# Performance work log

Measured on AMD Instinct MI355X. Metric: run time of the kernel, lower is better.

Reference implementation:

```python
import jax, jax.numpy as jnp
import numpy as np

B, H, N, F = 64, 24, 32, 256

def setup_inputs() -> dict:
    key = jax.random.key(0)
    ks = jax.random.split(key, 6)
    s = 1.0 / np.sqrt(F)
    return {
        "Q": jax.random.normal(ks[0], (B, N, F), jnp.float32),
        "K": jax.random.normal(ks[1], (B, H, N, F), jnp.float32),
        "V": jax.random.normal(ks[2], (B, H, N, F), jnp.float32),
        "Wq": jax.random.normal(ks[3], (N, F, F), jnp.float32) * s,
        "bq": jnp.zeros((N, F), jnp.float32),
        "Wk": jax.random.normal(ks[4], (N, H, F, F), jnp.float32) * s,
        "bk": jnp.zeros((N, H, F), jnp.float32),
        "Wv": jax.random.normal(ks[5], (N, H, F, F), jnp.float32) * s,
        "bv": jnp.zeros((N, H, F), jnp.float32),
    }

def reference(Q, K, V, Wq, bq, Wk, bk, Wv, bv):
    # Per-node query projection: [B,N,F]
    QWq = jnp.einsum('bnf,nfg->bng', Q, Wq) + bq
    # Per-node, per-encoder-step key/value projections: [B,N,H,F]
    KWk = jnp.einsum('bhnf,nhfg->bnhg', K, Wk) + bk
    VWv = jnp.einsum('bhnf,nhfg->bnhg', V, Wv) + bv
    # Attention scores over the H encoder steps (no sqrt(F) scaling, as in source)
    logits = jnp.einsum('bng,bnhg->bnh', QWq, KWk)
    scores = jax.nn.softmax(logits, axis=-1)          # [B,N,H]
    heads = jnp.einsum('bnh,bnhg->bng', scores, VWv)  # [B,N,F]
    return heads, scores
```

## Files before the change

### kernel.cpp

```cpp
#include <hip/hip_runtime.h>

typedef __attribute__((ext_vector_type(8))) short short8;
typedef __attribute__((ext_vector_type(4))) float f32x4;

#define B_ 64
#define H_ 24
#define N_ 32
#define F_ 256

__device__ __forceinline__ float bf2f(unsigned short u) {
    return __uint_as_float(((unsigned)u) << 16);
}
__device__ __forceinline__ unsigned short f2bf(float f) {
    unsigned u = __float_as_uint(f);
    u += 0x7fffu + ((u >> 16) & 1u);
    return (unsigned short)(u >> 16);
}
__device__ __forceinline__ unsigned pack_hi(float f0, float f1) {
    return (__float_as_uint(f0) >> 16) | (__float_as_uint(f1) & 0xffff0000u);
}
__device__ __forceinline__ float res_lo(float f) {
    return f - __uint_as_float(__float_as_uint(f) & 0xffff0000u);
}

struct StageT {
    unsigned short Ah[64 * 32];
    unsigned short Al[64 * 32];
    unsigned short Wh[256 * 32];
    unsigned short Wl[256 * 32];
};
union Smem {
    StageT t;
    unsigned short outT[64 * 256];
};

template<bool SPLIT>
__device__ __forceinline__ void gemm_f32(
    const float* __restrict__ Ab, long rstride,
    const float* __restrict__ Wb, Smem& sm, f32x4 acc[4][4])
{
    const int t    = threadIdx.x;
    const int lane = t & 63;
    const int wv   = t >> 6;
    const int l15  = lane & 15;
    const int quad = lane >> 4;
    const int arow = t >> 2, achk = (t & 3) * 8;
    const float* aSrc = Ab + (long)arow * rstride + achk;

    for (int ks = 0; ks < 8; ks++) {
        const int k0 = ks * 32;
        __syncthreads();
        {
            float4 a0 = *(const float4*)(aSrc + k0);
            float4 a1 = *(const float4*)(aSrc + k0 + 4);
            uint4 h;
            h.x = pack_hi(a0.x, a0.y); h.y = pack_hi(a0.z, a0.w);
            h.z = pack_hi(a1.x, a1.y); h.w = pack_hi(a1.z, a1.w);
            *(uint4*)&sm.t.Ah[arow * 32 + achk] = h;
            if (SPLIT) {
                uint4 l;
                l.x = pack_hi(res_lo(a0.x), res_lo(a0.y));
                l.y = pack_hi(res_lo(a0.z), res_lo(a0.w));
                l.z = pack_hi(res_lo(a1.x), res_lo(a1.y));
                l.w = pack_hi(res_lo(a1.z), res_lo(a1.w));
                *(uint4*)&sm.t.Al[arow * 32 + achk] = l;
            }
        }
        {
            union F4 { float4 v; float e[4]; } r[8];
            const float* wrow = Wb + (long)(k0 + wv * 8) * 256 + lane * 4;
            #pragma unroll
            for (int i = 0; i < 8; i++) r[i].v = *(const float4*)(wrow + i * 256);
            const int pos = wv ^ (lane & 3);
            #pragma unroll
            for (int j = 0; j < 4; j++) {
                uint4 h;
                h.x = pack_hi(r[0].e[j], r[1].e[j]);
                h.y = pack_hi(r[2].e[j], r[3].e[j]);
                h.z = pack_hi(r[4].e[j], r[5].e[j]);
                h.w = pack_hi(r[6].e[j], r[7].e[j]);
                *(uint4*)&sm.t.Wh[(lane * 4 + j) * 32 + pos * 8] = h;
                if (SPLIT) {
                    uint4 l;
                    l.x = pack_hi(res_lo(r[0].e[j]), res_lo(r[1].e[j]));
                    l.y = pack_hi(res_lo(r[2].e[j]), res_lo(r[3].e[j]));
                    l.z = pack_hi(res_lo(r[4].e[j]), res_lo(r[5].e[j]));
                    l.w = pack_hi(res_lo(r[6].e[j]), res_lo(r[7].e[j]));
                    *(uint4*)&sm.t.Wl[(lane * 4 + j) * 32 + pos * 8] = l;
                }
            }
        }
        __syncthreads();
        short8 ah[4], bh[4];
        #pragma unroll
        for (int mi = 0; mi < 4; mi++)
            ah[mi] = *(const short8*)&sm.t.Ah[(mi * 16 + l15) * 32 + quad * 8];
        const int bpos = quad ^ ((l15 >> 2) & 3);
        #pragma unroll
        for (int ni = 0; ni < 4; ni++) {
            int g = wv * 64 + ni * 16 + l15;
            bh[ni] = *(const short8*)&sm.t.Wh[g * 32 + bpos * 8];
        }
        if (SPLIT) {
            short8 al[4], bl[4];
            #pragma unroll
            for (int mi = 0; mi < 4; mi++)
                al[mi] = *(const short8*)&sm.t.Al[(mi * 16 + l15) * 32 + quad * 8];
            #pragma unroll
            for (int ni = 0; ni < 4; ni++) {
                int g = wv * 64 + ni * 16 + l15;
                bl[ni] = *(const short8*)&sm.t.Wl[g * 32 + bpos * 8];
            }
            #pragma unroll
            for (int mi = 0; mi < 4; mi++)
                #pragma unroll
                for (int ni = 0; ni < 4; ni++) {
                    acc[mi][ni] = __builtin_amdgcn_mfma_f32_16x16x32_bf16(al[mi], bh[ni], acc[mi][ni], 0, 0, 0);
                    acc[mi][ni] = __builtin_amdgcn_mfma_f32_16x16x32_bf16(ah[mi], bl[ni], acc[mi][ni], 0, 0, 0);
                    acc[mi][ni] = __builtin_amdgcn_mfma_f32_16x16x32_bf16(ah[mi], bh[ni], acc[mi][ni], 0, 0, 0);
                }
        } else {
            #pragma unroll
            for (int mi = 0; mi < 4; mi++)
                #pragma unroll
                for (int ni = 0; ni < 4; ni++)
                    acc[mi][ni] = __builtin_amdgcn_mfma_f32_16x16x32_bf16(ah[mi], bh[ni], acc[mi][ni], 0, 0, 0);
        }
    }
}

__global__ __launch_bounds__(256) void k_qproj(
    const float* __restrict__ Q, const float* __restrict__ Wq,
    const float* __restrict__ bq, float* __restrict__ qws)
{
    const int n = blockIdx.x;
    __shared__ Smem sm;
    f32x4 acc[4][4];
    #pragma unroll
    for (int i = 0; i < 4; i++)
        #pragma unroll
        for (int j = 0; j < 4; j++) acc[i][j] = (f32x4){0.f, 0.f, 0.f, 0.f};

    gemm_f32<true>(Q + n * F_, (long)(N_ * F_), Wq + (long)n * F_ * F_, sm, acc);

    const int t = threadIdx.x, lane = t & 63, wv = t >> 6;
    const int l15 = lane & 15, quad = lane >> 4;
    const float* bias = bq + n * F_;
    float* dst = qws + (long)n * (B_ * F_);
    #pragma unroll
    for (int ni = 0; ni < 4; ni++) {
        int g = wv * 64 + ni * 16 + l15;
        float bb = bias[g];
        #pragma unroll
        for (int mi = 0; mi < 4; mi++)
            #pragma unroll
            for (int reg = 0; reg < 4; reg++) {
                int r = mi * 16 + quad * 4 + reg;
                dst[r * 256 + g] = acc[mi][ni][reg] + bb;
            }
    }
}

__global__ __launch_bounds__(256) void k_kvproj(
    const float* __restrict__ Kx, const float* __restrict__ Vx,
    const float* __restrict__ Wk, const float* __restrict__ bk,
    const float* __restrict__ Wv, const float* __restrict__ bv,
    const float* __restrict__ qws, float* __restrict__ logits,
    unsigned short* __restrict__ vws)
{
    const int nh = blockIdx.x;
    const int n = nh / H_;
    const int h = nh - n * H_;
    const bool isV = (blockIdx.y != 0);
    const float* X    = isV ? Vx : Kx;
    const float* W    = (isV ? Wv : Wk) + (long)nh * F_ * F_;
    const float* bias = (isV ? bv : bk) + nh * F_;

    __shared__ Smem sm;
    __shared__ float slog[64];
    const int t = threadIdx.x;
    if (!isV && t < 64) slog[t] = 0.f;

    f32x4 acc[4][4];
    #pragma unroll
    for (int i = 0; i < 4; i++)
        #pragma unroll
        for (int j = 0; j < 4; j++) acc[i][j] = (f32x4){0.f, 0.f, 0.f, 0.f};

    if (isV) gemm_f32<false>(X + (long)(h * N_ + n) * F_, (long)(H_ * N_ * F_), W, sm, acc);
    else     gemm_f32<true >(X + (long)(h * N_ + n) * F_, (long)(H_ * N_ * F_), W, sm, acc);

    const int lane = t & 63, wv = t >> 6, l15 = lane & 15, quad = lane >> 4;

    if (!isV) {
        const float* qrow = qws + (long)n * (B_ * F_);
        #pragma unroll
        for (int mi = 0; mi < 4; mi++) {
            float p[4] = {0.f, 0.f, 0.f, 0.f};
            #pragma unroll
            for (int ni = 0; ni < 4; ni++) {
                int g = wv * 64 + ni * 16 + l15;
                float bb = bias[g];
                #pragma unroll
                for (int reg = 0; reg < 4; reg++) {
                    int r = mi * 16 + quad * 4 + reg;
                    p[reg] += (acc[mi][ni][reg] + bb) * qrow[r * 256 + g];
                }
            }
            #pragma unroll
            for (int off = 1; off < 16; off <<= 1)
                #pragma unroll
                for (int reg = 0; reg < 4; reg++)
                    p[reg] += __shfl_xor(p[reg], off, 64);
            if (l15 == 0)
                #pragma unroll
                for (int reg = 0; reg < 4; reg++)
                    atomicAdd(&slog[mi * 16 + quad * 4 + reg], p[reg]);
        }
        __syncthreads();
        if (t < 64) logits[(long)nh * 64 + t] = slog[t];
    } else {
        __syncthreads();
        #pragma unroll
        for (int ni = 0; ni < 4; ni++) {
            int g = wv * 64 + ni * 16 + l15;
            float bb = bias[g];
            #pragma unroll
            for (int mi = 0; mi < 4; mi++)
                #pragma unroll
                for (int reg = 0; reg < 4; reg++) {
                    int r = mi * 16 + quad * 4 + reg;
                    sm.outT[r * 256 + g] = f2bf(acc[mi][ni][reg] + bb);
                }
        }
        __syncthreads();
        unsigned short* dst = vws + (long)nh * (B_ * F_);
        #pragma unroll
        for (int it = 0; it < 8; it++) {
            int row = it * 8 + (t >> 5);
            int c = t & 31;
            uint4 v = *(const uint4*)(&sm.outT[row * 256 + c * 8]);
            *(uint4*)(dst + row * 256 + c * 8) = v;
        }
    }
}

__global__ __launch_bounds__(64) void k_attn(
    const float* __restrict__ logits,
    const unsigned short* __restrict__ vws,
    float* __restrict__ out)
{
    const int bx = blockIdx.x;
    const int b = bx >> 5;
    const int n = bx & 31;
    const int t = threadIdx.x;
    __shared__ float sl[24], se[24];
    if (t < 24) sl[t] = logits[(long)(n * H_ + t) * 64 + b];
    __syncthreads();
    float mx = -1e30f;
    #pragma unroll
    for (int h = 0; h < H_; h++) mx = fmaxf(mx, sl[h]);
    if (t < 24) se[t] = expf(sl[t] - mx);
    __syncthreads();
    float den = 0.f;
    #pragma unroll
    for (int h = 0; h < H_; h++) den += se[h];
    float inv = 1.0f / den;
    if (t < 24)
        out[(long)B_ * N_ * F_ + (long)(b * N_ + n) * H_ + t] = se[t] * inv;

    const int g0 = t * 4;
    float hv[4] = {0.f, 0.f, 0.f, 0.f};
    #pragma unroll
    for (int h = 0; h < H_; h++) {
        float s = se[h] * inv;
        const unsigned short* vp = vws + (((long)(n * H_ + h) * 64 + b) << 8) + g0;
        union { uint2 u; unsigned short e[4]; } vv;
        vv.u = *(const uint2*)vp;
        #pragma unroll
        for (int j = 0; j < 4; j++) hv[j] += s * bf2f(vv.e[j]);
    }
    float4 ov = make_float4(hv[0], hv[1], hv[2], hv[3]);
    *(float4*)(out + ((long)b * N_ + n) * F_ + g0) = ov;
}

extern "C" void kernel_launch(void* const* d_in, const int* in_sizes, int n_in,
                              void* d_out, int out_size, void* d_ws, size_t ws_size,
                              hipStream_t stream) {
    const float* Q  = (const float*)d_in[0];
    const float* K  = (const float*)d_in[1];
    const float* V  = (const float*)d_in[2];
    const float* Wq = (const float*)d_in[3];
    const float* bq = (const float*)d_in[4];
    const float* Wk = (const float*)d_in[5];
    const float* bk = (const float*)d_in[6];
    const float* Wv = (const float*)d_in[7];
    const float* bv = (const float*)d_in[8];

    char* ws = (char*)d_ws;
    float* qws          = (float*)ws;
    float* logits       = (float*)(ws + 2097152);
    unsigned short* vws = (unsigned short*)(ws + 2097152 + 262144);

    k_qproj<<<N_, 256, 0, stream>>>(Q, Wq, bq, qws);
    k_kvproj<<<dim3(N_ * H_, 2), 256, 0, stream>>>(K, V, Wk, bk, Wv, bv, qws, logits, vws);
    k_attn<<<B_ * N_, 64, 0, stream>>>(logits, vws, (float*)d_out);
}
```

Before: 495.7 us.

## Load GEMM operands directly from global into MFMA registers, dropping LDS staging

The LDS-staged GEMM is replaced with one where each wave loads its A and W fragments straight from global memory into registers, splits them to bf16, and feeds the MFMAs with no shared memory and no block barriers. The Q projection is split across 4 single-wave blocks per node, giving more blocks for the small launch. The aim is to remove the LDS round-trip and the per-k-step syncthreads. The cost is scalar, strided 4-byte W loads (8 rows per fragment), and every wave in a block re-reads the same A rows, which may reduce coalescing and raise global traffic.

Result: slower. 521.8 us (+5.3%).

```diff
diff --git a/kernel.cpp b/kernel.cpp
--- a/kernel.cpp
+++ b/kernel.cpp
@@ -23,127 +23,87 @@
     return f - __uint_as_float(__float_as_uint(f) & 0xffff0000u);
 }
 
-struct StageT {
-    unsigned short Ah[64 * 32];
-    unsigned short Al[64 * 32];
-    unsigned short Wh[256 * 32];
-    unsigned short Wl[256 * 32];
-};
-union Smem {
-    StageT t;
-    unsigned short outT[64 * 256];
-};
+union U4S8 { uint4 u; short8 s; };
 
 template<bool SPLIT>
-__device__ __forceinline__ void gemm_f32(
+__device__ __forceinline__ void gemm_direct(
     const float* __restrict__ Ab, long rstride,
-    const float* __restrict__ Wb, Smem& sm, f32x4 acc[4][4])
-{
-    const int t    = threadIdx.x;
-    const int lane = t & 63;
-    const int wv   = t >> 6;
+    const float* __restrict__ Wb, int wv, int lane,
+    f32x4 acc[4][4])
+{
     const int l15  = lane & 15;
     const int quad = lane >> 4;
-    const int arow = t >> 2, achk = (t & 3) * 8;
-    const float* aSrc = Ab + (long)arow * rstride + achk;
-
+    const float* abase = Ab + (long)l15 * rstride + quad * 8;
+    const float* wbase = Wb + (quad * 8) * F_ + wv * 64 + l15;
+
+    #pragma unroll
     for (int ks = 0; ks < 8; ks++) {
         const int k0 = ks * 32;
-        __syncthreads();
-        {
-            float4 a0 = *(const float4*)(aSrc + k0);
-            float4 a1 = *(const float4*)(aSrc + k0 + 4);
-            uint4 h;
-            h.x = pack_hi(a0.x, a0.y); h.y = pack_hi(a0.z, a0.w);
-            h.z = pack_hi(a1.x, a1.y); h.w = pack_hi(a1.z, a1.w);
-            *(uint4*)&sm.t.Ah[arow * 32 + achk] = h;
+        short8 ah[4], al[4];
+        #pragma unroll
+        for (int mi = 0; mi < 4; mi++) {
+            const float* ap = abase + (long)(mi * 16) * rstride + k0;
+            float4 a0 = *(const float4*)ap;
+            float4 a1 = *(const float4*)(ap + 4);
+            U4S8 h;
+            h.u.x = pack_hi(a0.x, a0.y); h.u.y = pack_hi(a0.z, a0.w);
+            h.u.z = pack_hi(a1.x, a1.y); h.u.w = pack_hi(a1.z, a1.w);
+            ah[mi] = h.s;
             if (SPLIT) {
-                uint4 l;
-                l.x = pack_hi(res_lo(a0.x), res_lo(a0.y));
-                l.y = pack_hi(res_lo(a0.z), res_lo(a0.w));
-                l.z = pack_hi(res_lo(a1.x), res_lo(a1.y));
-                l.w = pack_hi(res_lo(a1.z), res_lo(a1.w));
-                *(uint4*)&sm.t.Al[arow * 32 + achk] = l;
-            }
-        }
-        {
-            union F4 { float4 v; float e[4]; } r[8];
-            const float* wrow = Wb + (long)(k0 + wv * 8) * 256 + lane * 4;
-            #pragma unroll
-            for (int i = 0; i < 8; i++) r[i].v = *(const float4*)(wrow + i * 256);
-            const int pos = wv ^ (lane & 3);
-            #pragma unroll
-            for (int j = 0; j < 4; j++) {
-                uint4 h;
-                h.x = pack_hi(r[0].e[j], r[1].e[j]);
-                h.y = pack_hi(r[2].e[j], r[3].e[j]);
-                h.z = pack_hi(r[4].e[j], r[5].e[j]);
-                h.w = pack_hi(r[6].e[j], r[7].e[j]);
-                *(uint4*)&sm.t.Wh[(lane * 4 + j) * 32 + pos * 8] = h;
-                if (SPLIT) {
-                    uint4 l;
-                    l.x = pack_hi(res_lo(r[0].e[j]), res_lo(r[1].e[j]));
-                    l.y = pack_hi(res_lo(r[2].e[j]), res_lo(r[3].e[j]));
-                    l.z = pack_hi(res_lo(r[4].e[j]), res_lo(r[5].e[j]));
-                    l.w = pack_hi(res_lo(r[6].e[j]), res_lo(r[7].e[j]));
-                    *(uint4*)&sm.t.Wl[(lane * 4 + j) * 32 + pos * 8] = l;
+                U4S8 l;
+                l.u.x = pack_hi(res_lo(a0.x), res_lo(a0.y));
+                l.u.y = pack_hi(res_lo(a0.z), res_lo(a0.w));
+                l.u.z = pack_hi(res_lo(a1.x), res_lo(a1.y));
+                l.u.w = pack_hi(res_lo(a1.z), res_lo(a1.w));
+                al[mi] = l.s;
+            }
+        }
+        #pragma unroll
+        for (int ni = 0; ni < 4; ni++) {
+            const float* wp = wbase + (long)k0 * F_ + ni * 16;
+            float w[8];
+            #pragma unroll
+            for (int j = 0; j < 8; j++) w[j] = wp[j * F_];
+            U4S8 bh;
+            bh.u.x = pack_hi(w[0], w[1]); bh.u.y = pack_hi(w[2], w[3]);
+            bh.u.z = pack_hi(w[4], w[5]); bh.u.w = pack_hi(w[6], w[7]);
+            if (SPLIT) {
+                U4S8 bl;
+                bl.u.x = pack_hi(res_lo(w[0]), res_lo(w[1]));
+                bl.u.y = pack_hi(res_lo(w[2]), res_lo(w[3]));
+                bl.u.z = pack_hi(res_lo(w[4]), res_lo(w[5]));
+                bl.u.w = pack_hi(res_lo(w[6]), res_lo(w[7]));
+                #pragma unroll
+                for (int mi = 0; mi < 4; mi++) {
+                    acc[mi][ni] = __builtin_amdgcn_mfma_f32_16x16x32_bf16(al[mi], bh.s, acc[mi][ni], 0, 0, 0);
+                    acc[mi][ni] = __builtin_amdgcn_mfma_f32_16x16x32_bf16(ah[mi], bl.s, acc[mi][ni], 0, 0, 0);
+                    acc[mi][ni] = __builtin_amdgcn_mfma_f32_16x16x32_bf16(ah[mi], bh.s, acc[mi][ni], 0, 0, 0);
                 }
-            }
-        }
-        __syncthreads();
-        short8 ah[4], bh[4];
-        #pragma unroll
-        for (int mi = 0; mi < 4; mi++)
-            ah[mi] = *(const short8*)&sm.t.Ah[(mi * 16 + l15) * 32 + quad * 8];
-        const int bpos = quad ^ ((l15 >> 2) & 3);
-        #pragma unroll
-        for (int ni = 0; ni < 4; ni++) {
-            int g = wv * 64 + ni * 16 + l15;
-            bh[ni] = *(const short8*)&sm.t.Wh[g * 32 + bpos * 8];
-        }
-        if (SPLIT) {
-            short8 al[4], bl[4];
-            #pragma unroll
-            for (int mi = 0; mi < 4; mi++)
-                al[mi] = *(const short8*)&sm.t.Al[(mi * 16 + l15) * 32 + quad * 8];
-            #pragma unroll
-            for (int ni = 0; ni < 4; ni++) {
-                int g = wv * 64 + ni * 16 + l15;
-                bl[ni] = *(const short8*)&sm.t.Wl[g * 32 + bpos * 8];
-            }
-            #pragma unroll
-            for (int mi = 0; mi < 4; mi++)
-                #pragma unroll
-                for (int ni = 0; ni < 4; ni++) {
-                    acc[mi][ni] = __builtin_amdgcn_mfma_f32_16x16x32_bf16(al[mi], bh[ni], acc[mi][ni], 0, 0, 0);
-                    acc[mi][ni] = __builtin_amdgcn_mfma_f32_16x16x32_bf16(ah[mi], bl[ni], acc[mi][ni], 0, 0, 0);
-                    acc[mi][ni] = __builtin_amdgcn_mfma_f32_16x16x32_bf16(ah[mi], bh[ni], acc[mi][ni], 0, 0, 0);
-                }
-        } else {
-            #pragma unroll
-            for (int mi = 0; mi < 4; mi++)
-                #pragma unroll
-                for (int ni = 0; ni < 4; ni++)
-                    acc[mi][ni] = __builtin_amdgcn_mfma_f32_16x16x32_bf16(ah[mi], bh[ni], acc[mi][ni], 0, 0, 0);
-        }
-    }
-}
-
-__global__ __launch_bounds__(256) void k_qproj(
+            } else {
+                #pragma unroll
+                for (int mi = 0; mi < 4; mi++)
+                    acc[mi][ni] = __builtin_amdgcn_mfma_f32_16x16x32_bf16(ah[mi], bh.s, acc[mi][ni], 0, 0, 0);
+            }
+        }
+    }
+}
+
+__global__ __launch_bounds__(64) void k_qproj(
     const float* __restrict__ Q, const float* __restrict__ Wq,
     const float* __restrict__ bq, float* __restrict__ qws)
 {
-    const int n = blockIdx.x;
-    __shared__ Smem sm;
+    const int n  = blockIdx.x;
+    const int wv = blockIdx.y;
+    const int lane = threadIdx.x;
     f32x4 acc[4][4];
     #pragma unroll
     for (int i = 0; i < 4; i++)
         #pragma unroll
         for (int j = 0; j < 4; j++) acc[i][j] = (f32x4){0.f, 0.f, 0.f, 0.f};
 
-    gemm_f32<true>(Q + n * F_, (long)(N_ * F_), Wq + (long)n * F_ * F_, sm, acc);
-
-    const int t = threadIdx.x, lane = t & 63, wv = t >> 6;
+    gemm_direct<true>(Q + n * F_, (long)(N_ * F_), Wq + (long)n * F_ * F_,
+                      wv, lane, acc);
+
     const int l15 = lane & 15, quad = lane >> 4;
     const float* bias = bq + n * F_;
     float* dst = qws + (long)n * (B_ * F_);
@@ -176,7 +136,7 @@
     const float* W    = (isV ? Wv : Wk) + (long)nh * F_ * F_;
     const float* bias = (isV ? bv : bk) + nh * F_;
 
-    __shared__ Smem sm;
+    __shared__ unsigned short outT[64 * 256];
     __shared__ float slog[64];
     const int t = threadIdx.x;
     if (!isV && t < 64) slog[t] = 0.f;
@@ -187,12 +147,14 @@
         #pragma unroll
         for (int j = 0; j < 4; j++) acc[i][j] = (f32x4){0.f, 0.f, 0.f, 0.f};
 
-    if (isV) gemm_f32<false>(X + (long)(h * N_ + n) * F_, (long)(H_ * N_ * F_), W, sm, acc);
-    else     gemm_f32<true >(X + (long)(h * N_ + n) * F_, (long)(H_ * N_ * F_), W, sm, acc);
+    const float* Xb = X + (long)(h * N_ + n) * F_;
+    if (isV) gemm_direct<false>(Xb, (long)(H_ * N_ * F_), W, t >> 6, t & 63, acc);
+    else     gemm_direct<true >(Xb, (long)(H_ * N_ * F_), W, t >> 6, t & 63, acc);
 
     const int lane = t & 63, wv = t >> 6, l15 = lane & 15, quad = lane >> 4;
 
     if (!isV) {
+        __syncthreads();
         const float* qrow = qws + (long)n * (B_ * F_);
         #pragma unroll
         for (int mi = 0; mi < 4; mi++) {
@@ -220,7 +182,6 @@
         __syncthreads();
         if (t < 64) logits[(long)nh * 64 + t] = slog[t];
     } else {
-        __syncthreads();
         #pragma unroll
         for (int ni = 0; ni < 4; ni++) {
             int g = wv * 64 + ni * 16 + l15;
@@ -230,7 +191,7 @@
                 #pragma unroll
                 for (int reg = 0; reg < 4; reg++) {
                     int r = mi * 16 + quad * 4 + reg;
-                    sm.outT[r * 256 + g] = f2bf(acc[mi][ni][reg] + bb);
+                    outT[r * 256 + g] = f2bf(acc[mi][ni][reg] + bb);
                 }
         }
         __syncthreads();
@@ -239,7 +200,7 @@
         for (int it = 0; it < 8; it++) {
             int row = it * 8 + (t >> 5);
             int c = t & 31;
-            uint4 v = *(const uint4*)(&sm.outT[row * 256 + c * 8]);
+            uint4 v = *(const uint4*)(&outT[row * 256 + c * 8]);
             *(uint4*)(dst + row * 256 + c * 8) = v;
         }
     }
@@ -302,7 +263,7 @@
     float* logits       = (float*)(ws + 2097152);
     unsigned short* vws = (unsigned short*)(ws + 2097152 + 262144);
 
-    k_qproj<<<N_, 256, 0, stream>>>(Q, Wq, bq, qws);
+    k_qproj<<<dim3(N_, 4), 64, 0, stream>>>(Q, Wq, bq, qws);
     k_kvproj<<<dim3(N_ * H_, 2), 256, 0, stream>>>(K, V, Wk, bk, Wv, bv, qws, logits, vws);
     k_attn<<<B_ * N_, 64, 0, stream>>>(logits, vws, (float*)d_out);
 }
```

## Prefetch next K-slice into registers during MFMA and reorder B-fragment loads

Applied to the files above, without the earlier changes.

The GEMM loop now issues the global loads for the next 32-wide K slice of A and W into registers right after the LDS barrier, so they overlap with the MFMA work on the current slice (register double-buffering). The MFMA loop is reordered to load B fragments one column tile at a time, which cuts live short8 registers. Both kernels also get a launch-bounds minimum of 3 blocks per CU. In exchange, the prefetch buffers raise register pressure, and the occupancy hint may force spills.

Result: no change. 496.4 us (+0.1%).

```diff
diff --git a/kernel.cpp b/kernel.cpp
--- a/kernel.cpp
+++ b/kernel.cpp
@@ -46,13 +46,22 @@
     const int quad = lane >> 4;
     const int arow = t >> 2, achk = (t & 3) * 8;
     const float* aSrc = Ab + (long)arow * rstride + achk;
-
+    const float* wSrc = Wb + (long)(wv * 8) * 256 + lane * 4;
+    const int pos  = wv ^ (lane & 3);
+    const int bpos = quad ^ ((l15 >> 2) & 3);
+
+    union F4 { float4 v; float e[4]; };
+
+    float4 a0 = *(const float4*)(aSrc);
+    float4 a1 = *(const float4*)(aSrc + 4);
+    F4 r[8];
+    #pragma unroll
+    for (int i = 0; i < 8; i++) r[i].v = *(const float4*)(wSrc + i * 256);
+
+    #pragma unroll
     for (int ks = 0; ks < 8; ks++) {
-        const int k0 = ks * 32;
         __syncthreads();
         {
-            float4 a0 = *(const float4*)(aSrc + k0);
-            float4 a1 = *(const float4*)(aSrc + k0 + 4);
             uint4 h;
             h.x = pack_hi(a0.x, a0.y); h.y = pack_hi(a0.z, a0.w);
             h.z = pack_hi(a1.x, a1.y); h.w = pack_hi(a1.z, a1.w);
@@ -65,71 +74,75 @@
                 l.w = pack_hi(res_lo(a1.z), res_lo(a1.w));
                 *(uint4*)&sm.t.Al[arow * 32 + achk] = l;
             }
+            #pragma unroll
+            for (int j = 0; j < 4; j++) {
+                uint4 hh;
+                hh.x = pack_hi(r[0].e[j], r[1].e[j]);
+                hh.y = pack_hi(r[2].e[j], r[3].e[j]);
+                hh.z = pack_hi(r[4].e[j], r[5].e[j]);
+                hh.w = pack_hi(r[6].e[j], r[7].e[j]);
+                *(uint4*)&sm.t.Wh[(lane * 4 + j) * 32 + pos * 8] = hh;
+                if (SPLIT) {
+                    uint4 ll;
+                    ll.x = pack_hi(res_lo(r[0].e[j]), res_lo(r[1].e[j]));
+                    ll.y = pack_hi(res_lo(r[2].e[j]), res_lo(r[3].e[j]));
+                    ll.z = pack_hi(res_lo(r[4].e[j]), res_lo(r[5].e[j]));
+                    ll.w = pack_hi(res_lo(r[6].e[j]), res_lo(r[7].e[j]));
+                    *(uint4*)&sm.t.Wl[(lane * 4 + j) * 32 + pos * 8] = ll;
+                }
+            }
+        }
+        __syncthreads();
+        float4 na0, na1;
+        F4 nr[8];
+        if (ks < 7) {
+            const int k1 = (ks + 1) * 32;
+            na0 = *(const float4*)(aSrc + k1);
+            na1 = *(const float4*)(aSrc + k1 + 4);
+            #pragma unroll
+            for (int i = 0; i < 8; i++)
+                nr[i].v = *(const float4*)(wSrc + k1 * 256 + i * 256);
         }
         {
-            union F4 { float4 v; float e[4]; } r[8];
-            const float* wrow = Wb + (long)(k0 + wv * 8) * 256 + lane * 4;
-            #pragma unroll
-            for (int i = 0; i < 8; i++) r[i].v = *(const float4*)(wrow + i * 256);
-            const int pos = wv ^ (lane & 3);
-            #pragma unroll
-            for (int j = 0; j < 4; j++) {
-                uint4 h;
-                h.x = pack_hi(r[0].e[j], r[1].e[j]);
-                h.y = pack_hi(r[2].e[j], r[3].e[j]);
-                h.z = pack_hi(r[4].e[j], r[5].e[j]);
-                h.w = pack_hi(r[6].e[j], r[7].e[j]);
-                *(uint4*)&sm.t.Wh[(lane * 4 + j) * 32 + pos * 8] = h;
-                if (SPLIT) {
-                    uint4 l;
-                    l.x = pack_hi(res_lo(r[0].e[j]), res_lo(r[1].e[j]));
-                    l.y = pack_hi(res_lo(r[2].e[j]), res_lo(r[3].e[j]));
-                    l.z = pack_hi(res_lo(r[4].e[j]), res_lo(r[5].e[j]));
-                    l.w = pack_hi(res_lo(r[6].e[j]), res_lo(r[7].e[j]));
-                    *(uint4*)&sm.t.Wl[(lane * 4 + j) * 32 + pos * 8] = l;
-                }
-            }
-        }
-        __syncthreads();
-        short8 ah[4], bh[4];
-        #pragma unroll
-        for (int mi = 0; mi < 4; mi++)
-            ah[mi] = *(const short8*)&sm.t.Ah[(mi * 16 + l15) * 32 + quad * 8];
-        const int bpos = quad ^ ((l15 >> 2) & 3);
-        #pragma unroll
-        for (int ni = 0; ni < 4; ni++) {
-            int g = wv * 64 + ni * 16 + l15;
-            bh[ni] = *(const short8*)&sm.t.Wh[g * 32 + bpos * 8];
-        }
-        if (SPLIT) {
-            short8 al[4], bl[4];
+            short8 ah[4];
             #pragma unroll
             for (int mi = 0; mi < 4; mi++)
-                al[mi] = *(const short8*)&sm.t.Al[(mi * 16 + l15) * 32 + quad * 8];
-            #pragma unroll
-            for (int ni = 0; ni < 4; ni++) {
-                int g = wv * 64 + ni * 16 + l15;
-                bl[ni] = *(const short8*)&sm.t.Wl[g * 32 + bpos * 8];
-            }
-            #pragma unroll
-            for (int mi = 0; mi < 4; mi++)
+                ah[mi] = *(const short8*)&sm.t.Ah[(mi * 16 + l15) * 32 + quad * 8];
+            if (SPLIT) {
+                short8 al[4];
+                #pragma unroll
+                for (int mi = 0; mi < 4; mi++)
+                    al[mi] = *(const short8*)&sm.t.Al[(mi * 16 + l15) * 32 + quad * 8];
                 #pragma unroll
                 for (int ni = 0; ni < 4; ni++) {
-                    acc[mi][ni] = __builtin_amdgcn_mfma_f32_16x16x32_bf16(al[mi], bh[ni], acc[mi][ni], 0, 0, 0);
-                    acc[mi][ni] = __builtin_amdgcn_mfma_f32_16x16x32_bf16(ah[mi], bl[ni], acc[mi][ni], 0, 0, 0);
-                    acc[mi][ni] = __builtin_amdgcn_mfma_f32_16x16x32_bf16(ah[mi], bh[ni], acc[mi][ni], 0, 0, 0);
-                }
-        } else {
-            #pragma unroll
-            for (int mi = 0; mi < 4; mi++)
-                #pragma unroll
-                for (int ni = 0; ni < 4; ni++)
-                    acc[mi][ni] = __builtin_amdgcn_mfma_f32_16x16x32_bf16(ah[mi], bh[ni], acc[mi][ni], 0, 0, 0);
-        }
+                    int g = wv * 64 + ni * 16 + l15;
+                    short8 bh = *(const short8*)&sm.t.Wh[g * 32 + bpos * 8];
+                    short8 bl = *(const short8*)&sm.t.Wl[g * 32 + bpos * 8];
+                    #pragma unroll
+                    for (int mi = 0; mi < 4; mi++) {
+                        acc[mi][ni] = __builtin_amdgcn_mfma_f32_16x16x32_bf16(al[mi], bh, acc[mi][ni], 0, 0, 0);
+                        acc[mi][ni] = __builtin_amdgcn_mfma_f32_16x16x32_bf16(ah[mi], bl, acc[mi][ni], 0, 0, 0);
+                        acc[mi][ni] = __builtin_amdgcn_mfma_f32_16x16x32_bf16(ah[mi], bh, acc[mi][ni], 0, 0, 0);
+                    }
+                }
+            } else {
+                #pragma unroll
+                for (int ni = 0; ni < 4; ni++) {
+                    int g = wv * 64 + ni * 16 + l15;
+                    short8 bh = *(const short8*)&sm.t.Wh[g * 32 + bpos * 8];
+                    #pragma unroll
+                    for (int mi = 0; mi < 4; mi++)
+                        acc[mi][ni] = __builtin_amdgcn_mfma_f32_16x16x32_bf16(ah[mi], bh, acc[mi][ni], 0, 0, 0);
+                }
+            }
+        }
+        a0 = na0; a1 = na1;
+        #pragma unroll
+        for (int i = 0; i < 8; i++) r[i] = nr[i];
     }
 }
 
-__global__ __launch_bounds__(256) void k_qproj(
+__global__ __launch_bounds__(256, 3) void k_qproj(
     const float* __restrict__ Q, const float* __restrict__ Wq,
     const float* __restrict__ bq, float* __restrict__ qws)
 {
@@ -161,7 +174,7 @@
     }
 }
 
-__global__ __launch_bounds__(256) void k_kvproj(
+__global__ __launch_bounds__(256, 3) void k_kvproj(
     const float* __restrict__ Kx, const float* __restrict__ Vx,
     const float* __restrict__ Wk, const float* __restrict__ bk,
     const float* __restrict__ Wv, const float* __restrict__ bv,
@@ -187,8 +200,9 @@
         #pragma unroll
         for (int j = 0; j < 4; j++) acc[i][j] = (f32x4){0.f, 0.f, 0.f, 0.f};
 
-    if (isV) gemm_f32<false>(X + (long)(h * N_ + n) * F_, (long)(H_ * N_ * F_), W, sm, acc);
-    else     gemm_f32<true >(X + (long)(h * N_ + n) * F_, (long)(H_ * N_ * F_), W, sm, acc);
+    const float* Xb = X + (long)(h * N_ + n) * F_;
+    if (isV) gemm_f32<false>(Xb, (long)(H_ * N_ * F_), W, sm, acc);
+    else     gemm_f32<true >(Xb, (long)(H_ * N_ * F_), W, sm, acc);
 
     const int lane = t & 63, wv = t >> 6, l15 = lane & 15, quad = lane >> 4;
 
```
